# Optimization experiments

Hardware: AMD Instinct MI355X
Metric: run time of the kernel (lower is better)

## Reference

```python
import jax, jax.numpy as jnp
import numpy as np

# bitsandbytes NF4 codebook (16 levels)
NF4 = jnp.array([-1.0, -0.6961928009986877, -0.5250730514526367, -0.39491748809814453,
                 -0.28444138169288635, -0.18477343022823334, -0.09105003625154495, 0.0,
                 0.07958029955625534, 0.16093020141124725, 0.24611230194568634,
                 0.33791524171829224, 0.44070982933044434, 0.5626170039176941,
                 0.7229568362236023, 1.0], dtype=jnp.float32)
BLOCK = 64  # NF4 quantization blocksize
HD, M, TOKENS = 4096, 11008, 512


def dequant_nf4(codes, absmax, out_f, in_f):
    # codes: int [out_f, in_f] in [0,16); absmax: float [out_f*in_f/BLOCK]
    w = NF4[codes.reshape(-1, BLOCK)] * absmax[:, None]
    return w.reshape(out_f, in_f)


def setup_inputs() -> dict:
    key = jax.random.key(0)
    ks = jax.random.split(key, 7)
    x = jax.random.normal(ks[0], (TOKENS, HD), dtype=jnp.float32)
    gate_codes = jax.random.randint(ks[1], (M, HD), 0, 16, dtype=jnp.int32)
    up_codes = jax.random.randint(ks[2], (M, HD), 0, 16, dtype=jnp.int32)
    down_codes = jax.random.randint(ks[3], (HD, M), 0, 16, dtype=jnp.int32)
    n_blk = (M * HD) // BLOCK
    gate_absmax = jax.random.uniform(ks[4], (n_blk,), dtype=jnp.float32) * 0.02 + 1e-3
    up_absmax = jax.random.uniform(ks[5], (n_blk,), dtype=jnp.float32) * 0.02 + 1e-3
    down_absmax = jax.random.uniform(ks[6], (n_blk,), dtype=jnp.float32) * 0.02 + 1e-3
    return {"x": x, "gate_codes": gate_codes, "gate_absmax": gate_absmax,
            "up_codes": up_codes, "up_absmax": up_absmax,
            "down_codes": down_codes, "down_absmax": down_absmax}


def reference(x, gate_codes, gate_absmax, up_codes, up_absmax, down_codes, down_absmax):
    # Dequantize NF4 weights on the fly, then SwiGLU MLP:
    # down( silu(gate(x)) * up(x) )
    Wg = dequant_nf4(gate_codes, gate_absmax, M, HD)   # [m, hd]
    Wu = dequant_nf4(up_codes, up_absmax, M, HD)       # [m, hd]
    Wd = dequant_nf4(down_codes, down_absmax, HD, M)   # [hd, m]
    g = x @ Wg.T                                       # [tokens, m]
    u = x @ Wu.T                                       # [tokens, m]
    h = jax.nn.silu(g) * u                             # [tokens, m]
    return h @ Wd.T                                    # [tokens, hd]
```

## Files before the change

kernel.cpp:

```cpp
#include <hip/hip_runtime.h>
#include <hip/hip_bf16.h>
#include <cstdint>
#include <cstddef>

#define TOKENS 512

using float4v = __attribute__((ext_vector_type(4))) float;
using short8  = __attribute__((ext_vector_type(8))) short;

__constant__ float NF4TAB[16] = {
  -1.0f, -0.6961928009986877f, -0.5250730514526367f, -0.39491748809814453f,
  -0.28444138169288635f, -0.18477343022823334f, -0.09105003625154495f, 0.0f,
  0.07958029955625534f, 0.16093020141124725f, 0.24611230194568634f,
  0.33791524171829224f, 0.44070982933044434f, 0.5626170039176941f,
  0.7229568362236023f, 1.0f };

__device__ __forceinline__ unsigned short f2bf(float f) {
  unsigned u = __float_as_uint(f);
  u += 0x7fffu + ((u >> 16) & 1u);
  return (unsigned short)(u >> 16);
}
__device__ __forceinline__ float bf2f(unsigned short b) {
  return __uint_as_float(((unsigned)b) << 16);
}

__device__ __forceinline__ void async16(const void* g, void* l) {
  __builtin_amdgcn_global_load_lds(
      (const __attribute__((address_space(1))) void*)g,
      (__attribute__((address_space(3))) void*)l, 16, 0, 0);
}

template <int EPI>
__global__ __launch_bounds__(256) void gemm_nf4(
    const unsigned short* __restrict__ A,
    const int* __restrict__ codes,
    const float* __restrict__ absmax,
    float* __restrict__ outF,
    unsigned short* __restrict__ outB,
    const unsigned short* __restrict__ gIn,
    int N, int K, int Kc, int Mtiles, int Ntiles)
{
  __shared__ unsigned short Abuf[256 * 64];
  __shared__ unsigned short Bbuf[64 * 72];
  __shared__ float tab[16];

  const int tid  = threadIdx.x;
  const int lane = tid & 63;
  const int wave = tid >> 6;

  if (tid < 16) tab[tid] = NF4TAB[tid];

  const int bid = blockIdx.x;
  const int mt  = bid % Mtiles;
  const int r1  = bid / Mtiles;
  const int nt  = r1 % Ntiles;
  const int ks  = r1 / Ntiles;

  const int row0 = mt * 256;
  const int col0 = nt * 64;
  const int k0   = ks * Kc;
  const int nk   = Kc >> 6;

  const int arow = lane >> 3;
  const int achk = (lane & 7) ^ arow;
  const unsigned short* aSrc0 =
      A + (size_t)(row0 + wave * 8 + arow) * K + k0 + achk * 8;

  const int bn = tid >> 2;
  const int bq = tid & 3;
  const int* cSrc = codes + (size_t)(col0 + bn) * K + k0;
  const float* amSrc = absmax + (size_t)(col0 + bn) * (K >> 6) + (k0 >> 6);

  float4v acc[4][4];
  {
    float4v z = {0.f, 0.f, 0.f, 0.f};
    #pragma unroll
    for (int i = 0; i < 4; ++i)
      #pragma unroll
      for (int j = 0; j < 4; ++j) acc[i][j] = z;
  }

  __syncthreads();

  for (int kt = 0; kt < nk; ++kt) {
    #pragma unroll
    for (int j = 0; j < 8; ++j) {
      async16(aSrc0 + (size_t)j * 32 * K + kt * 64,
              &Abuf[(j * 4 + wave) * 512]);
    }
    const float am = amSrc[kt];
    #pragma unroll
    for (int i = 0; i < 4; ++i) {
      int4 c4 = ((const int4*)(cSrc + kt * 64))[i * 4 + bq];
      ushort4 w;
      w.x = f2bf(tab[c4.x] * am);
      w.y = f2bf(tab[c4.y] * am);
      w.z = f2bf(tab[c4.z] * am);
      w.w = f2bf(tab[c4.w] * am);
      *(ushort4*)&Bbuf[bn * 72 + i * 16 + bq * 4] = w;
    }
    __syncthreads();

    #pragma unroll
    for (int kk = 0; kk < 2; ++kk) {
      short8 af[4], bfr[4];
      #pragma unroll
      for (int i = 0; i < 4; ++i) {
        const int row_l = wave * 64 + i * 16 + (lane & 15);
        const int gl    = kk * 4 + (lane >> 4);
        const int phys  = gl ^ (lane & 7);
        af[i] = *(const short8*)&Abuf[row_l * 64 + phys * 8];
      }
      #pragma unroll
      for (int j = 0; j < 4; ++j) {
        const int n_l = j * 16 + (lane & 15);
        bfr[j] = *(const short8*)&Bbuf[n_l * 72 + kk * 32 + (lane >> 4) * 8];
      }
      #pragma unroll
      for (int i = 0; i < 4; ++i)
        #pragma unroll
        for (int j = 0; j < 4; ++j)
          acc[i][j] = __builtin_amdgcn_mfma_f32_16x16x32_bf16(af[i], bfr[j], acc[i][j], 0, 0, 0);
    }
    __syncthreads();
  }

  const int ccol  = col0 + (lane & 15);
  const int crow0 = row0 + wave * 64 + ((lane >> 4) << 2);
  #pragma unroll
  for (int i = 0; i < 4; ++i) {
    #pragma unroll
    for (int j = 0; j < 4; ++j) {
      #pragma unroll
      for (int r = 0; r < 4; ++r) {
        const size_t idx = (size_t)(crow0 + i * 16 + r) * N + (ccol + j * 16);
        if (EPI == 2) {
          atomicAdd(&outF[idx], acc[i][j][r]);
        } else if (EPI == 0) {
          outB[idx] = f2bf(acc[i][j][r]);
        } else {
          const float gv = bf2f(gIn[idx]);
          const float s  = gv / (1.f + __expf(-gv));
          outB[idx] = f2bf(s * acc[i][j][r]);
        }
      }
    }
  }
}

__global__ void cast_bf16_kernel(const float* __restrict__ x,
                                 unsigned short* __restrict__ xb, int n4) {
  int i = blockIdx.x * blockDim.x + threadIdx.x;
  if (i < n4) {
    float4 v = ((const float4*)x)[i];
    ushort4 o;
    o.x = f2bf(v.x); o.y = f2bf(v.y); o.z = f2bf(v.z); o.w = f2bf(v.w);
    ((ushort4*)xb)[i] = o;
  }
}

extern "C" void kernel_launch(void* const* d_in, const int* in_sizes, int n_in,
                              void* d_out, int out_size, void* d_ws, size_t ws_size,
                              hipStream_t stream)
{
  (void)in_sizes; (void)n_in; (void)ws_size;
  const float* x            = (const float*)d_in[0];
  const int*   gate_codes   = (const int*)d_in[1];
  const float* gate_absmax  = (const float*)d_in[2];
  const int*   up_codes     = (const int*)d_in[3];
  const float* up_absmax    = (const float*)d_in[4];
  const int*   down_codes   = (const int*)d_in[5];
  const float* down_absmax  = (const float*)d_in[6];
  float* out = (float*)d_out;

  unsigned short* xb = (unsigned short*)d_ws;
  unsigned short* g  = xb + (size_t)512 * 4096;
  unsigned short* h  = g  + (size_t)512 * 11008;

  hipMemsetAsync(d_out, 0, (size_t)out_size * sizeof(float), stream);

  cast_bf16_kernel<<<2048, 256, 0, stream>>>(x, xb, (512 * 4096) / 4);

  gemm_nf4<0><<<344, 256, 0, stream>>>(xb, gate_codes, gate_absmax,
                                       nullptr, g, nullptr,
                                       11008, 4096, 4096, 2, 172);
  gemm_nf4<1><<<344, 256, 0, stream>>>(xb, up_codes, up_absmax,
                                       nullptr, h, g,
                                       11008, 4096, 4096, 2, 172);
  gemm_nf4<2><<<512, 256, 0, stream>>>(h, down_codes, down_absmax,
                                       out, nullptr, nullptr,
                                       4096, 11008, 2752, 2, 64);
}
```

Baseline: 761.8 us.

## Switch NF4 GEMMs to fp16 with paired-code table, register A loads, double-buffered B

Switches the whole pipeline from bf16 to fp16 MFMA. Dequantisation now goes through a 256-entry LUT that yields two fp16 weights per lookup, scaled with half2 multiplies. The A operand is read straight from global memory into registers instead of being staged in LDS, and B is double-buffered with codes prefetched two tiles ahead. Gate and up run in one launch of 688 blocks, with SwiGLU moved to a separate elementwise kernel. Tradeoffs: fp16 narrows the range for activations and g/u, the extra SwiGLU pass adds round-trip memory traffic, and uncached global A loads may stress bandwidth.

```diff
diff --git a/kernel.cpp b/kernel.cpp
--- a/kernel.cpp
+++ b/kernel.cpp
@@ -1,12 +1,11 @@
 #include <hip/hip_runtime.h>
-#include <hip/hip_bf16.h>
+#include <hip/hip_fp16.h>
 #include <cstdint>
 #include <cstddef>
 
-#define TOKENS 512
 
 using float4v = __attribute__((ext_vector_type(4))) float;
-using short8  = __attribute__((ext_vector_type(8))) short;
+using half8   = __attribute__((ext_vector_type(8))) _Float16;
 
 __constant__ float NF4TAB[16] = {
   -1.0f, -0.6961928009986877f, -0.5250730514526367f, -0.39491748809814453f,
@@ -15,61 +14,50 @@
   0.33791524171829224f, 0.44070982933044434f, 0.5626170039176941f,
   0.7229568362236023f, 1.0f };
 
-__device__ __forceinline__ unsigned short f2bf(float f) {
-  unsigned u = __float_as_uint(f);
-  u += 0x7fffu + ((u >> 16) & 1u);
-  return (unsigned short)(u >> 16);
-}
-__device__ __forceinline__ float bf2f(unsigned short b) {
-  return __uint_as_float(((unsigned)b) << 16);
-}
-
-__device__ __forceinline__ void async16(const void* g, void* l) {
-  __builtin_amdgcn_global_load_lds(
-      (const __attribute__((address_space(1))) void*)g,
-      (__attribute__((address_space(3))) void*)l, 16, 0, 0);
-}
-
-template <int EPI>
-__global__ __launch_bounds__(256) void gemm_nf4(
-    const unsigned short* __restrict__ A,
-    const int* __restrict__ codes,
-    const float* __restrict__ absmax,
+template <bool ATOMIC>
+__global__ __launch_bounds__(256, 2) void gemm_nf4(
+    const __half* __restrict__ Ag,
+    const int* __restrict__ c0, const float* __restrict__ am0,
+    const int* __restrict__ c1, const float* __restrict__ am1,
+    __half* __restrict__ o0, __half* __restrict__ o1,
     float* __restrict__ outF,
-    unsigned short* __restrict__ outB,
-    const unsigned short* __restrict__ gIn,
-    int N, int K, int Kc, int Mtiles, int Ntiles)
+    int N, int K, int Kc, int Ntiles)
 {
-  __shared__ unsigned short Abuf[256 * 64];
-  __shared__ unsigned short Bbuf[64 * 72];
-  __shared__ float tab[16];
+  __shared__ __half    Bb[2][64 * 72];
+  __shared__ unsigned  ptab[256];
 
   const int tid  = threadIdx.x;
   const int lane = tid & 63;
   const int wave = tid >> 6;
 
-  if (tid < 16) tab[tid] = NF4TAB[tid];
+  {
+    __half2 pr = __floats2half2_rn(NF4TAB[tid & 15], NF4TAB[tid >> 4]);
+    ptab[tid] = *(const unsigned*)&pr;
+  }
 
   const int bid = blockIdx.x;
-  const int mt  = bid % Mtiles;
-  const int r1  = bid / Mtiles;
-  const int nt  = r1 % Ntiles;
-  const int ks  = r1 / Ntiles;
+  const int mt  = bid & 1;
+  const int r   = bid >> 1;
+  const int nt  = r % Ntiles;
+  const int r2  = r / Ntiles;
+
+  const int k0 = ATOMIC ? r2 * Kc : 0;
+  const int nk = Kc >> 6;
+  const int* codes   = (!ATOMIC && r2) ? c1 : c0;
+  const float* amax  = (!ATOMIC && r2) ? am1 : am0;
+  __half* outH       = (!ATOMIC && r2) ? o1 : o0;
 
   const int row0 = mt * 256;
   const int col0 = nt * 64;
-  const int k0   = ks * Kc;
-  const int nk   = Kc >> 6;
-
-  const int arow = lane >> 3;
-  const int achk = (lane & 7) ^ arow;
-  const unsigned short* aSrc0 =
-      A + (size_t)(row0 + wave * 8 + arow) * K + k0 + achk * 8;
+  const int Kb   = K >> 6;
 
   const int bn = tid >> 2;
   const int bq = tid & 3;
-  const int* cSrc = codes + (size_t)(col0 + bn) * K + k0;
-  const float* amSrc = absmax + (size_t)(col0 + bn) * (K >> 6) + (k0 >> 6);
+  const int4* cSrc   = (const int4*)(codes + (size_t)(col0 + bn) * K + k0);
+  const float* amSrc = amax + (size_t)(col0 + bn) * Kb + (k0 >> 6);
+
+  const __half* aBase = Ag + (size_t)(row0 + wave * 64 + (lane & 15)) * K
+                           + k0 + ((lane >> 4) << 3);
 
   float4v acc[4][4];
   {
@@ -80,82 +68,113 @@
       for (int j = 0; j < 4; ++j) acc[i][j] = z;
   }
 
+  int4  cr[2][4];
+  float amr[2];
+  half8 apf[2][4];
+
+#define LOADC(S, KT)                                                            \
+  { const int4* _p = cSrc + (KT) * 16;                                          \
+    cr[S][0] = _p[bq];      cr[S][1] = _p[4 + bq];                              \
+    cr[S][2] = _p[8 + bq];  cr[S][3] = _p[12 + bq];                             \
+    amr[S] = amSrc[KT]; }
+
+#define DEQB(BUFI, S)                                                           \
+  { const __half _ah = __float2half(amr[S]);                                    \
+    const __half2 _am2 = __half2{_ah, _ah};                                     \
+    _Pragma("unroll")                                                           \
+    for (int _i = 0; _i < 4; ++_i) {                                            \
+      unsigned _w0 = ptab[cr[S][_i].x | (cr[S][_i].y << 4)];                    \
+      unsigned _w1 = ptab[cr[S][_i].z | (cr[S][_i].w << 4)];                    \
+      __half2 _p0 = __hmul2(*(const __half2*)&_w0, _am2);                       \
+      __half2 _p1 = __hmul2(*(const __half2*)&_w1, _am2);                       \
+      uint2 _wv; _wv.x = *(const unsigned*)&_p0; _wv.y = *(const unsigned*)&_p1;\
+      *(uint2*)&Bb[BUFI][bn * 72 + _i * 16 + bq * 4] = _wv; } }
+
+#define LOADA(DST, KT, KK)                                                      \
+  { _Pragma("unroll")                                                           \
+    for (int _i = 0; _i < 4; ++_i)                                              \
+      DST[_i] = *(const half8*)(aBase + (size_t)_i * 16 * K + (KT) * 64 + (KK) * 32); }
+
+  LOADC(0, 0);
+  if (nk > 1) LOADC(1, 1);
   __syncthreads();
-
-  for (int kt = 0; kt < nk; ++kt) {
-    #pragma unroll
-    for (int j = 0; j < 8; ++j) {
-      async16(aSrc0 + (size_t)j * 32 * K + kt * 64,
-              &Abuf[(j * 4 + wave) * 512]);
-    }
-    const float am = amSrc[kt];
-    #pragma unroll
-    for (int i = 0; i < 4; ++i) {
-      int4 c4 = ((const int4*)(cSrc + kt * 64))[i * 4 + bq];
-      ushort4 w;
-      w.x = f2bf(tab[c4.x] * am);
-      w.y = f2bf(tab[c4.y] * am);
-      w.z = f2bf(tab[c4.z] * am);
-      w.w = f2bf(tab[c4.w] * am);
-      *(ushort4*)&Bbuf[bn * 72 + i * 16 + bq * 4] = w;
-    }
-    __syncthreads();
-
-    #pragma unroll
-    for (int kk = 0; kk < 2; ++kk) {
-      short8 af[4], bfr[4];
-      #pragma unroll
-      for (int i = 0; i < 4; ++i) {
-        const int row_l = wave * 64 + i * 16 + (lane & 15);
-        const int gl    = kk * 4 + (lane >> 4);
-        const int phys  = gl ^ (lane & 7);
-        af[i] = *(const short8*)&Abuf[row_l * 64 + phys * 8];
-      }
-      #pragma unroll
-      for (int j = 0; j < 4; ++j) {
-        const int n_l = j * 16 + (lane & 15);
-        bfr[j] = *(const short8*)&Bbuf[n_l * 72 + kk * 32 + (lane >> 4) * 8];
-      }
-      #pragma unroll
-      for (int i = 0; i < 4; ++i)
-        #pragma unroll
-        for (int j = 0; j < 4; ++j)
-          acc[i][j] = __builtin_amdgcn_mfma_f32_16x16x32_bf16(af[i], bfr[j], acc[i][j], 0, 0, 0);
-    }
-    __syncthreads();
-  }
-
-  const int ccol  = col0 + (lane & 15);
+  DEQB(0, 0);
+  if (nk > 2) LOADC(0, 2);
+  LOADA(apf[0], 0, 0);
+  __syncthreads();
+
+#define BODY(KT, S)                                                             \
+  { const int _np = (S) ^ 1;                                                    \
+    if ((KT) + 1 < nk) {                                                        \
+      DEQB(_np, _np);                            \
+      if ((KT) + 3 < nk) LOADC(_np, (KT) + 3);                                  \
+      LOADA(apf[_np], (KT) + 1, 0);                                             \
+    }                                                                           \
+    half8 a1[4];                                                                \
+    LOADA(a1, KT, 1);              \
+    half8 bf[4];                                                                \
+    _Pragma("unroll")                                                           \
+    for (int _j = 0; _j < 4; ++_j)                                              \
+      bf[_j] = *(const half8*)&Bb[S][(_j * 16 + (lane & 15)) * 72 + ((lane >> 4) << 3)]; \
+    _Pragma("unroll")                                                           \
+    for (int _i = 0; _i < 4; ++_i)                                              \
+      _Pragma("unroll")                                                         \
+      for (int _j = 0; _j < 4; ++_j)                                            \
+        acc[_i][_j] = __builtin_amdgcn_mfma_f32_16x16x32_f16(apf[S][_i], bf[_j], acc[_i][_j], 0, 0, 0); \
+    _Pragma("unroll")                                                           \
+    for (int _j = 0; _j < 4; ++_j)                                              \
+      bf[_j] = *(const half8*)&Bb[S][(_j * 16 + (lane & 15)) * 72 + 32 + ((lane >> 4) << 3)]; \
+    _Pragma("unroll")                                                           \
+    for (int _i = 0; _i < 4; ++_i)                                              \
+      _Pragma("unroll")                                                         \
+      for (int _j = 0; _j < 4; ++_j)                                            \
+        acc[_i][_j] = __builtin_amdgcn_mfma_f32_16x16x32_f16(a1[_i], bf[_j], acc[_i][_j], 0, 0, 0); \
+    __syncthreads(); }
+
+  int kt = 0;
+  while (kt + 2 <= nk) { BODY(kt, 0); BODY(kt + 1, 1); kt += 2; }
+  if (kt < nk) BODY(kt, 0);
+
+  const int ccol0 = col0 + (lane & 15);
   const int crow0 = row0 + wave * 64 + ((lane >> 4) << 2);
   #pragma unroll
-  for (int i = 0; i < 4; ++i) {
+  for (int i = 0; i < 4; ++i)
     #pragma unroll
-    for (int j = 0; j < 4; ++j) {
+    for (int j = 0; j < 4; ++j)
       #pragma unroll
-      for (int r = 0; r < 4; ++r) {
-        const size_t idx = (size_t)(crow0 + i * 16 + r) * N + (ccol + j * 16);
-        if (EPI == 2) {
-          atomicAdd(&outF[idx], acc[i][j][r]);
-        } else if (EPI == 0) {
-          outB[idx] = f2bf(acc[i][j][r]);
-        } else {
-          const float gv = bf2f(gIn[idx]);
-          const float s  = gv / (1.f + __expf(-gv));
-          outB[idx] = f2bf(s * acc[i][j][r]);
-        }
+      for (int rr = 0; rr < 4; ++rr) {
+        const size_t idx = (size_t)(crow0 + i * 16 + rr) * N + (ccol0 + j * 16);
+        if (ATOMIC) atomicAdd(&outF[idx], acc[i][j][rr]);
+        else        outH[idx] = __float2half(acc[i][j][rr]);
       }
-    }
-  }
-}
-
-__global__ void cast_bf16_kernel(const float* __restrict__ x,
-                                 unsigned short* __restrict__ xb, int n4) {
+#undef LOADC
+#undef DEQB
+#undef LOADA
+#undef BODY
+}
+
+__global__ void cast_f16_kernel(const float* __restrict__ x,
+                                __half* __restrict__ xh, int n4) {
   int i = blockIdx.x * blockDim.x + threadIdx.x;
   if (i < n4) {
     float4 v = ((const float4*)x)[i];
-    ushort4 o;
-    o.x = f2bf(v.x); o.y = f2bf(v.y); o.z = f2bf(v.z); o.w = f2bf(v.w);
-    ((ushort4*)xb)[i] = o;
+    __half2 h0 = __floats2half2_rn(v.x, v.y);
+    __half2 h1 = __floats2half2_rn(v.z, v.w);
+    ((__half2*)xh)[2 * i]     = h0;
+    ((__half2*)xh)[2 * i + 1] = h1;
+  }
+}
+
+__global__ void swiglu_kernel(const __half* __restrict__ g,
+                              const __half* __restrict__ u,
+                              __half* __restrict__ h, int n2) {
+  int i = blockIdx.x * blockDim.x + threadIdx.x;
+  if (i < n2) {
+    float2 gf = __half22float2(((const __half2*)g)[i]);
+    float2 uf = __half22float2(((const __half2*)u)[i]);
+    float h0 = gf.x / (1.f + __expf(-gf.x)) * uf.x;
+    float h1 = gf.y / (1.f + __expf(-gf.y)) * uf.y;
+    ((__half2*)h)[i] = __floats2half2_rn(h0, h1);
   }
 }
 
@@ -173,21 +192,22 @@
   const float* down_absmax  = (const float*)d_in[6];
   float* out = (float*)d_out;
 
-  unsigned short* xb = (unsigned short*)d_ws;
-  unsigned short* g  = xb + (size_t)512 * 4096;
-  unsigned short* h  = g  + (size_t)512 * 11008;
+  __half* xh = (__half*)d_ws;
+  __half* g  = xh + (size_t)512 * 4096;
+  __half* u  = g  + (size_t)512 * 11008;
 
   hipMemsetAsync(d_out, 0, (size_t)out_size * sizeof(float), stream);
 
-  cast_bf16_kernel<<<2048, 256, 0, stream>>>(x, xb, (512 * 4096) / 4);
-
-  gemm_nf4<0><<<344, 256, 0, stream>>>(xb, gate_codes, gate_absmax,
-                                       nullptr, g, nullptr,
-                                       11008, 4096, 4096, 2, 172);
-  gemm_nf4<1><<<344, 256, 0, stream>>>(xb, up_codes, up_absmax,
-                                       nullptr, h, g,
-                                       11008, 4096, 4096, 2, 172);
-  gemm_nf4<2><<<512, 256, 0, stream>>>(h, down_codes, down_absmax,
-                                       out, nullptr, nullptr,
-                                       4096, 11008, 2752, 2, 64);
-}
+  cast_f16_kernel<<<2048, 256, 0, stream>>>(x, xh, (512 * 4096) / 4);
+
+  gemm_nf4<false><<<688, 256, 0, stream>>>(xh, gate_codes, gate_absmax,
+                                           up_codes, up_absmax,
+                                           g, u, nullptr,
+                                           11008, 4096, 4096, 172);
+
+  swiglu_kernel<<<11008, 256, 0, stream>>>(g, u, g, (512 * 11008) / 2);
+
+  gemm_nf4<true><<<512, 256, 0, stream>>>(g, down_codes, down_absmax,
+                                          nullptr, nullptr, nullptr, nullptr,
+                                          out, 4096, 11008, 2752, 64);
+}
```

New measurement: 864.8 us. 13.5% more time.
